# Performance work log

Measured on AMD Instinct MI355X. Metric: run time of the kernel, lower is better.

The kernel has to match this reference:

```python
import jax, jax.numpy as jnp
import numpy as np

NB_CLASSES = 10
EPS = 1e-8  # torch cosine_similarity eps


def gcn_conv(x, W, b, src, dst, n):
    h = x @ W
    deg = jax.ops.segment_sum(jnp.ones_like(src, dtype=h.dtype), dst, num_segments=n) + 1.0
    dinv = deg ** -0.5
    coef = (dinv[src] * dinv[dst])[:, None]
    agg = jax.ops.segment_sum(h[src] * coef, dst, num_segments=n)
    return agg + h * (1.0 / deg)[:, None] + b


def condition_net(e, w_in, b_in, w_hid, b_hid, w_out, b_out):
    # ConditionNet with num_layers=2: input_fc -> elu -> hidden_fc[0] -> elu -> output_fc
    h = jax.nn.elu(e @ w_in + b_in)
    h = jax.nn.elu(h @ w_hid + b_hid)
    return h @ w_out + b_out


def setup_inputs() -> dict:
    key = jax.random.key(0)
    N, E, D, H, T, M = 20000, 320000, 256, 256, 3, 2048
    ks = jax.random.split(key, 24)
    s = 1.0 / np.sqrt(D)
    inp = {
        "x": jax.random.normal(ks[0], (N, D), dtype=jnp.float32),
        "src": jax.random.randint(ks[1], (E,), 0, N, dtype=jnp.int32),
        "dst": jax.random.randint(ks[2], (E,), 0, N, dtype=jnp.int32),
        "idx": jax.random.randint(ks[3], (M,), 0, N, dtype=jnp.int32),
        "labels": jax.random.randint(ks[4], (M,), 0, NB_CLASSES, dtype=jnp.int32),
        "train": 1,
        # 3 GCNConv layers (all D->D, residual structure forces equal widths)
        "gcn_W1": jax.random.normal(ks[5], (D, D), dtype=jnp.float32) * s,
        "gcn_b1": jnp.zeros((D,), dtype=jnp.float32),
        "gcn_W2": jax.random.normal(ks[6], (D, D), dtype=jnp.float32) * s,
        "gcn_b2": jnp.zeros((D,), dtype=jnp.float32),
        "gcn_W3": jax.random.normal(ks[7], (D, D), dtype=jnp.float32) * s,
        "gcn_b3": jnp.zeros((D,), dtype=jnp.float32),
        # T=3 ConditionNets, params stacked on leading axis
        "cn_w_in": jax.random.normal(ks[8], (T, D, H), dtype=jnp.float32) * s,
        "cn_b_in": jnp.zeros((T, H), dtype=jnp.float32),
        "cn_w_hid": jax.random.normal(ks[9], (T, H, H), dtype=jnp.float32) * s,
        "cn_b_hid": jnp.zeros((T, H), dtype=jnp.float32),
        "cn_w_out": jax.random.normal(ks[10], (T, H, D), dtype=jnp.float32) * s,
        "cn_b_out": jnp.zeros((T, D), dtype=jnp.float32),
        # Embed_prompt
        "p_list": jax.random.normal(ks[11], (5, D), dtype=jnp.float32) * s,
        "a_W": jax.random.normal(ks[12], (D, 5), dtype=jnp.float32) * s,
        "a_b": jnp.zeros((5,), dtype=jnp.float32),
        # gcn_weight2 (trainable); weight1 and weight3 are frozen zeros, closed over
        "gcn_weight2": jnp.float32(1.0),
    }
    return inp


def reference(x, src, dst, idx, labels, train,
              gcn_W1, gcn_b1, gcn_W2, gcn_b2, gcn_W3, gcn_b3,
              cn_w_in, cn_b_in, cn_w_hid, cn_b_hid, cn_w_out, cn_b_out,
              p_list, a_W, a_b, gcn_weight2):
    n = x.shape[0]
    origin_x = x
    w1 = jnp.float32(0.0)  # gcn_weight1 (frozen)
    w3 = jnp.float32(0.0)  # gcn_weight3 (frozen)
    T = cn_w_in.shape[0]
    for t in range(T):  # think layers (small static count)
        e1 = gcn_conv(x, gcn_W1, gcn_b1, src, dst, n)
        e2 = gcn_conv(e1, gcn_W2, gcn_b2, src, dst, n) + e1
        e3 = gcn_conv(e2, gcn_W3, gcn_b3, src, dst, n) + e2
        embed = w1 * e1 + gcn_weight2 * e2 + w3 * e3
        prompt = condition_net(embed, cn_w_in[t], cn_b_in[t], cn_w_hid[t], cn_b_hid[t],
                               cn_w_out[t], cn_b_out[t])
        x = prompt * origin_x
    # full gcn(x, edge_index): 3 convs with ELU activation (standard GCN forward)
    h = jax.nn.elu(gcn_conv(x, gcn_W1, gcn_b1, src, dst, n))
    h = jax.nn.elu(gcn_conv(h, gcn_W2, gcn_b2, src, dst, n))
    h = jax.nn.elu(gcn_conv(h, gcn_W3, gcn_b3, src, dst, n))
    # Embed_prompt: attention over 5 learned prompt vectors
    weight = jax.nn.softmax(h @ a_W + a_b, axis=1)  # [N, 5]
    embed = h + weight @ p_list
    rawret = embed[idx]  # [M, D]
    # train==1: class prototypes via scatter-mean over labels
    sums = jax.ops.segment_sum(rawret, labels, num_segments=NB_CLASSES)
    counts = jax.ops.segment_sum(jnp.ones_like(labels, dtype=rawret.dtype), labels,
                                 num_segments=NB_CLASSES)
    ave = sums / jnp.maximum(counts, 1.0)[:, None]  # [C, D]
    # fused cosine similarity: normalize both, one matmul (replaces M*C scalar loop)
    rn = rawret / jnp.maximum(jnp.linalg.norm(rawret, axis=1, keepdims=True), EPS)
    an = ave / jnp.maximum(jnp.linalg.norm(ave, axis=1, keepdims=True), EPS)
    ret = jax.nn.softmax(rn @ an.T, axis=1)  # [M, C]
    return ret
```

## Files before the change

### kernel.cpp

```cpp
#include <hip/hip_runtime.h>
#include <hip/hip_bf16.h>
#include <math.h>

#define NN 20000
#define DD 256
#define EE 320000
#define MM 2048
#define CC 10
#define TT 3

typedef __attribute__((ext_vector_type(8))) short s8v;
typedef __attribute__((ext_vector_type(4))) float f4v;

__device__ unsigned short g_xb[NN * DD];
__device__ unsigned short g_xo[NN * DD];
__device__ unsigned short g_hb[NN * DD];
__device__ unsigned short g_e1b[NN * DD];
__device__ unsigned short g_e2b[NN * DD];
__device__ int   g_cnt[NN];
__device__ int   g_cursor[NN];
__device__ int   g_rowstart[NN + 1];
__device__ float g_dinv[NN];
__device__ float g_invdeg[NN];
__device__ int   g_part[128];
__device__ int2  g_edge[EE];
__device__ float g_sums[CC * DD];
__device__ float g_cntf[CC];
__device__ float g_an[CC * DD];
__device__ unsigned short g_wT1[12 * DD * DD];
__device__ unsigned short g_wT2[12 * DD * DD];

__device__ __forceinline__ float wave_sum(float v) {
#pragma unroll
  for (int off = 32; off > 0; off >>= 1) v += __shfl_xor(v, off);
  return v;
}

__device__ __forceinline__ float eluf(float x) {
  return x > 0.f ? x : expm1f(x);
}

__device__ __forceinline__ float bf2f(unsigned short u) {
  union { unsigned int i; float f; } c;
  c.i = (unsigned int)u << 16;
  return c.f;
}

__device__ __forceinline__ float2 bfpair(unsigned int d) {
  union { unsigned int i; float f; } a, b;
  a.i = d << 16;
  b.i = d & 0xffff0000u;
  return make_float2(a.f, b.f);
}

__device__ __forceinline__ unsigned int packbf(float x, float y) {
  union { __hip_bfloat162 v; unsigned int u; } c;
  c.v = __float22bfloat162_rn(make_float2(x, y));
  return c.u;
}

__device__ __forceinline__ void gl_lds16(const unsigned short* g, unsigned short* l) {
  __builtin_amdgcn_global_load_lds(
      (const __attribute__((address_space(1))) unsigned int*)g,
      (__attribute__((address_space(3))) unsigned int*)l, 16, 0, 0);
}

__global__ void zero_pre() {
  int i = blockIdx.x * blockDim.x + threadIdx.x;
  if (i < NN) { g_cnt[i] = 0; g_cursor[i] = 0; }
  if (i < CC * DD) g_sums[i] = 0.f;
  if (i < CC) g_cntf[i] = 0.f;
}

__global__ void hist_k(const int* __restrict__ dst) {
  int e = blockIdx.x * blockDim.x + threadIdx.x;
  if (e < EE) atomicAdd(&g_cnt[dst[e]], 1);
}

__global__ __launch_bounds__(256) void scanA_k() {
  __shared__ int s[256];
  int t = threadIdx.x;
  int i = blockIdx.x * 256 + t;
  int v = (i < NN) ? g_cnt[i] : 0;
  s[t] = v;
  __syncthreads();
#pragma unroll
  for (int off = 128; off > 0; off >>= 1) {
    if (t < off) s[t] += s[t + off];
    __syncthreads();
  }
  if (t == 0) g_part[blockIdx.x] = s[0];
}

__global__ __launch_bounds__(128) void scanB_k() {
  __shared__ int s[128];
  int t = threadIdx.x;
  int p = (t < 79) ? g_part[t] : 0;
  s[t] = p;
  __syncthreads();
#pragma unroll
  for (int off = 1; off < 128; off <<= 1) {
    int v = (t >= off) ? s[t - off] : 0;
    __syncthreads();
    s[t] += v;
    __syncthreads();
  }
  g_part[t] = s[t] - p;
  if (t == 0) g_rowstart[NN] = EE;
}

__global__ __launch_bounds__(256) void scanC_k() {
  __shared__ int s[256];
  int t = threadIdx.x;
  int i = blockIdx.x * 256 + t;
  int v = (i < NN) ? g_cnt[i] : 0;
  s[t] = v;
  __syncthreads();
#pragma unroll
  for (int off = 1; off < 256; off <<= 1) {
    int x = (t >= off) ? s[t - off] : 0;
    __syncthreads();
    s[t] += x;
    __syncthreads();
  }
  if (i < NN) {
    g_rowstart[i] = g_part[blockIdx.x] + s[t] - v;
    float dg = (float)(v + 1);
    g_invdeg[i] = 1.0f / dg;
    g_dinv[i] = 1.0f / sqrtf(dg);
  }
}

__global__ void fill_k(const int* __restrict__ src, const int* __restrict__ dst) {
  int e = blockIdx.x * blockDim.x + threadIdx.x;
  if (e < EE) {
    int d = dst[e];
    int p = atomicAdd(&g_cursor[d], 1);
    int j = g_rowstart[d] + p;
    int si = src[e];
    float coef = g_dinv[si] * g_dinv[d];
    g_edge[j] = make_int2(si * 512, __float_as_int(coef));
  }
}

__global__ __launch_bounds__(256) void cvt_k(const float* __restrict__ x,
                                             unsigned short* __restrict__ xb) {
  int i = blockIdx.x * blockDim.x + threadIdx.x;
  const float4* x4 = (const float4*)x;
  float4 a = x4[i * 2], b = x4[i * 2 + 1];
  uint4 o;
  o.x = packbf(a.x, a.y);
  o.y = packbf(a.z, a.w);
  o.z = packbf(b.x, b.y);
  o.w = packbf(b.z, b.w);
  ((uint4*)xb)[i] = o;
}

struct WPtrs { const float* p[12]; };

__global__ __launch_bounds__(256) void wprep_k(WPtrs wp) {
  __shared__ float t[64][65];
  int widx = blockIdx.z;
  int kt0 = blockIdx.x * 64, nt0 = blockIdx.y * 64;
  const float* W = wp.p[widx];
  int tid = threadIdx.x;
  int ln = tid & 63, lk = tid >> 6;
  for (int kk = lk; kk < 64; kk += 4)
    t[kk][ln] = W[(size_t)(kt0 + kk) * DD + nt0 + ln];
  __syncthreads();
  for (int nn = lk; nn < 64; nn += 4) {
    float v = t[ln][nn];
    __hip_bfloat16 hb = __float2bfloat16(v);
    float hf = __bfloat162float(hb);
    __hip_bfloat16 lb = __float2bfloat16(v - hf);
    union { __hip_bfloat16 b; unsigned short s; } ch, cl;
    ch.b = hb; cl.b = lb;
    size_t o = (size_t)widx * DD * DD + (size_t)(nt0 + nn) * DD + kt0 + ln;
    g_wT1[o] = ch.s;
    g_wT2[o] = cl.s;
  }
}

union GemmSM {
  unsigned short st[2 * 2048 * 8];
  float ct[128][68];
};

template <int EPI>
__global__ __launch_bounds__(256) void gemm_k(const unsigned short* __restrict__ A,
                                              const unsigned short* __restrict__ B1,
                                              const unsigned short* __restrict__ B2,
                                              unsigned short* __restrict__ C,
                                              const float* __restrict__ bias,
                                              const float* __restrict__ alphap,
                                              const unsigned short* __restrict__ mul) {
  __shared__ GemmSM sm;
  int b = blockIdx.x;
  int xcd = b & 7, off = b >> 3;
  int logical = (xcd < 4) ? xcd * 79 + off : 316 + (xcd - 4) * 78 + off;
  int mblk = logical >> 2, nblk = logical & 3;
  int row0 = mblk * 128, col0 = nblk * 64;

  int tid = threadIdx.x;
  int wv = tid >> 6, lane = tid & 63;
  int wm = wv >> 1, wn = wv & 1;
  int lr = lane & 15, lk = lane >> 4;

  f4v acc[4][2];
#pragma unroll
  for (int i = 0; i < 4; ++i)
#pragma unroll
    for (int j = 0; j < 2; ++j) acc[i][j] = (f4v){0.f, 0.f, 0.f, 0.f};

  auto stage = [&](int buf, int kt) {
    unsigned short* base = sm.st + buf * 16384;
#pragma unroll
    for (int i = 0; i < 8; ++i) {
      int cb = (wv * 8 + i) * 64;
      int c = cb + lane;
      unsigned short* ldst = base + (size_t)cb * 8;
      if (cb < 1024) {
        int row = c >> 3, kc = c & 7;
        int gr = row0 + row;
        gr = gr < NN ? gr : NN - 1;
        gl_lds16(A + (size_t)gr * DD + kt + ((kc ^ (row & 7)) << 3), ldst);
      } else if (cb < 1536) {
        int c2 = c - 1024;
        int col = c2 >> 3, kc = c2 & 7;
        gl_lds16(B1 + (size_t)(col0 + col) * DD + kt + ((kc ^ (col & 7)) << 3), ldst);
      } else {
        int c2 = c - 1536;
        int col = c2 >> 3, kc = c2 & 7;
        gl_lds16(B2 + (size_t)(col0 + col) * DD + kt + ((kc ^ (col & 7)) << 3), ldst);
      }
    }
  };

  stage(0, 0);
  __syncthreads();

  int buf = 0;
#pragma unroll
  for (int t = 0; t < 4; ++t) {
    if (t < 3) stage(buf ^ 1, (t + 1) * 64);
    const unsigned short* base = sm.st + buf * 16384;
#pragma unroll
    for (int ksub = 0; ksub < 2; ++ksub) {
      int kc = ksub * 4 + lk;
      s8v a[4], b1v[2], b2v[2];
#pragma unroll
      for (int mi = 0; mi < 4; ++mi) {
        int row = wm * 64 + mi * 16 + lr;
        a[mi] = *(const s8v*)(base + (row * 8 + (kc ^ (row & 7))) * 8);
      }
#pragma unroll
      for (int nj = 0; nj < 2; ++nj) {
        int col = wn * 32 + nj * 16 + lr;
        int ch = col * 8 + (kc ^ (col & 7));
        b1v[nj] = *(const s8v*)(base + 8192 + ch * 8);
        b2v[nj] = *(const s8v*)(base + 12288 + ch * 8);
      }
#pragma unroll
      for (int mi = 0; mi < 4; ++mi)
#pragma unroll
        for (int nj = 0; nj < 2; ++nj) {
          acc[mi][nj] = __builtin_amdgcn_mfma_f32_16x16x32_bf16(a[mi], b1v[nj], acc[mi][nj], 0, 0, 0);
          acc[mi][nj] = __builtin_amdgcn_mfma_f32_16x16x32_bf16(a[mi], b2v[nj], acc[mi][nj], 0, 0, 0);
        }
    }
    __syncthreads();
    buf ^= 1;
  }

#pragma unroll
  for (int mi = 0; mi < 4; ++mi)
#pragma unroll
    for (int nj = 0; nj < 2; ++nj)
#pragma unroll
      for (int r = 0; r < 4; ++r)
        sm.ct[wm * 64 + mi * 16 + lk * 4 + r][wn * 32 + nj * 16 + lr] = acc[mi][nj][r];
  __syncthreads();

  float alpha = 1.f;
  if (EPI == 1) alpha = alphap ? *alphap : 1.f;
#pragma unroll
  for (int p = 0; p < 4; ++p) {
    int row = p * 32 + (tid >> 3);
    int c0 = (tid & 7) * 8;
    int gr = row0 + row;
    int gc = col0 + c0;
    if (gr < NN) {
      float v[8];
      float4 va = *(float4*)&sm.ct[row][c0];
      float4 vb = *(float4*)&sm.ct[row][c0 + 4];
      v[0] = va.x; v[1] = va.y; v[2] = va.z; v[3] = va.w;
      v[4] = vb.x; v[5] = vb.y; v[6] = vb.z; v[7] = vb.w;
      if (EPI == 1) {
        float4 bv0 = *(const float4*)(bias + gc);
        float4 bv1 = *(const float4*)(bias + gc + 4);
        float bb[8] = {bv0.x, bv0.y, bv0.z, bv0.w, bv1.x, bv1.y, bv1.z, bv1.w};
#pragma unroll
        for (int i = 0; i < 8; ++i) v[i] = eluf(fmaf(alpha, v[i], bb[i]));
      } else if (EPI == 2) {
        float4 bv0 = *(const float4*)(bias + gc);
        float4 bv1 = *(const float4*)(bias + gc + 4);
        float bb[8] = {bv0.x, bv0.y, bv0.z, bv0.w, bv1.x, bv1.y, bv1.z, bv1.w};
        uint4 mu = *(const uint4*)(mul + (size_t)gr * DD + gc);
        float2 m0 = bfpair(mu.x), m1 = bfpair(mu.y), m2 = bfpair(mu.z), m3 = bfpair(mu.w);
        float mm[8] = {m0.x, m0.y, m1.x, m1.y, m2.x, m2.y, m3.x, m3.y};
#pragma unroll
        for (int i = 0; i < 8; ++i) v[i] = (v[i] + bb[i]) * mm[i];
      }
      uint4 o;
      o.x = packbf(v[0], v[1]);
      o.y = packbf(v[2], v[3]);
      o.z = packbf(v[4], v[5]);
      o.w = packbf(v[6], v[7]);
      *(uint4*)(C + (size_t)gr * DD + gc) = o;
    }
  }
}

template <int RES>
__device__ __forceinline__ float4 agg_row_b(int row, int lane,
                                            const unsigned short* __restrict__ h,
                                            const float* __restrict__ bias,
                                            const unsigned short* __restrict__ res) {
  const char* hb = (const char*)h;
  int lo = lane * 8;
  float4 a = make_float4(0.f, 0.f, 0.f, 0.f);
  int s = g_rowstart[row], e = g_rowstart[row + 1];
  int j = s;
  for (; j + 16 <= e; j += 16) {
    int2 E[16];
    uint2 v[16];
#pragma unroll
    for (int u = 0; u < 16; ++u) E[u] = g_edge[j + u];
#pragma unroll
    for (int u = 0; u < 16; ++u) v[u] = *(const uint2*)(hb + E[u].x + lo);
#pragma unroll
    for (int u = 0; u < 16; ++u) {
      float c = __int_as_float(E[u].y);
      float2 p0 = bfpair(v[u].x), p1 = bfpair(v[u].y);
      a.x = fmaf(c, p0.x, a.x); a.y = fmaf(c, p0.y, a.y);
      a.z = fmaf(c, p1.x, a.z); a.w = fmaf(c, p1.y, a.w);
    }
  }
  for (; j + 4 <= e; j += 4) {
    int2 E[4];
    uint2 v[4];
#pragma unroll
    for (int u = 0; u < 4; ++u) E[u] = g_edge[j + u];
#pragma unroll
    for (int u = 0; u < 4; ++u) v[u] = *(const uint2*)(hb + E[u].x + lo);
#pragma unroll
    for (int u = 0; u < 4; ++u) {
      float c = __int_as_float(E[u].y);
      float2 p0 = bfpair(v[u].x), p1 = bfpair(v[u].y);
      a.x = fmaf(c, p0.x, a.x); a.y = fmaf(c, p0.y, a.y);
      a.z = fmaf(c, p1.x, a.z); a.w = fmaf(c, p1.y, a.w);
    }
  }
  for (; j < e; ++j) {
    int2 E0 = g_edge[j];
    uint2 v0 = *(const uint2*)(hb + E0.x + lo);
    float c = __int_as_float(E0.y);
    float2 p0 = bfpair(v0.x), p1 = bfpair(v0.y);
    a.x = fmaf(c, p0.x, a.x); a.y = fmaf(c, p0.y, a.y);
    a.z = fmaf(c, p1.x, a.z); a.w = fmaf(c, p1.y, a.w);
  }
  float idg = g_invdeg[row];
  uint2 hv = *(const uint2*)(hb + row * 512 + lo);
  float2 h0 = bfpair(hv.x), h1 = bfpair(hv.y);
  float4 bv = ((const float4*)bias)[lane];
  float4 o;
  o.x = a.x + h0.x * idg + bv.x;
  o.y = a.y + h0.y * idg + bv.y;
  o.z = a.z + h1.x * idg + bv.z;
  o.w = a.w + h1.y * idg + bv.w;
  if (RES) {
    uint2 rv = *(const uint2*)((const char*)res + row * 512 + lo);
    float2 r0 = bfpair(rv.x), r1 = bfpair(rv.y);
    o.x += r0.x; o.y += r0.y; o.z += r1.x; o.w += r1.y;
  }
  return o;
}

template <int ELU, int RES>
__global__ __launch_bounds__(256) void agg_k(const unsigned short* __restrict__ h,
                                             const float* __restrict__ bias,
                                             const unsigned short* __restrict__ res,
                                             unsigned short* __restrict__ out) {
  int row = (blockIdx.x * 256 + threadIdx.x) >> 6;
  int lane = threadIdx.x & 63;
  float4 o = agg_row_b<RES>(row, lane, h, bias, res);
  if (ELU) {
    o.x = eluf(o.x); o.y = eluf(o.y); o.z = eluf(o.z); o.w = eluf(o.w);
  }
  ((uint2*)out)[(size_t)row * 64 + lane] = make_uint2(packbf(o.x, o.y), packbf(o.z, o.w));
}

__global__ __launch_bounds__(256) void aggattn_k(const unsigned short* __restrict__ h,
                                                 const float* __restrict__ bias,
                                                 const float* __restrict__ aW,
                                                 const float* __restrict__ ab,
                                                 const float* __restrict__ plist,
                                                 unsigned short* __restrict__ out) {
  int row = (blockIdx.x * 256 + threadIdx.x) >> 6;
  int lane = threadIdx.x & 63;
  float4 o = agg_row_b<0>(row, lane, h, bias, nullptr);
  o.x = eluf(o.x); o.y = eluf(o.y); o.z = eluf(o.z); o.w = eluf(o.w);
  int d = lane * 4;
  float lg[5];
#pragma unroll
  for (int k = 0; k < 5; ++k) {
    float p = o.x * aW[(d + 0) * 5 + k] + o.y * aW[(d + 1) * 5 + k] +
              o.z * aW[(d + 2) * 5 + k] + o.w * aW[(d + 3) * 5 + k];
    lg[k] = wave_sum(p) + ab[k];
  }
  float mx = lg[0];
#pragma unroll
  for (int k = 1; k < 5; ++k) mx = fmaxf(mx, lg[k]);
  float w[5], sum = 0.f;
#pragma unroll
  for (int k = 0; k < 5; ++k) { w[k] = expf(lg[k] - mx); sum += w[k]; }
  float inv = 1.f / sum;
#pragma unroll
  for (int k = 0; k < 5; ++k) {
    float wk = w[k] * inv;
    float4 pv = ((const float4*)plist)[k * 64 + lane];
    o.x = fmaf(wk, pv.x, o.x);
    o.y = fmaf(wk, pv.y, o.y);
    o.z = fmaf(wk, pv.z, o.z);
    o.w = fmaf(wk, pv.w, o.w);
  }
  ((uint2*)out)[(size_t)row * 64 + lane] = make_uint2(packbf(o.x, o.y), packbf(o.z, o.w));
}

__global__ __launch_bounds__(256) void proto_k(const unsigned short* __restrict__ embed,
                                               const int* __restrict__ idxp,
                                               const int* __restrict__ labels) {
  __shared__ float sums[CC][DD];
  __shared__ float cnts[CC];
  int t = threadIdx.x;
#pragma unroll
  for (int c = 0; c < CC; ++c) sums[c][t] = 0.f;
  if (t < CC) cnts[t] = 0.f;
  __syncthreads();
  int m0 = blockIdx.x * 32;
  for (int r0 = 0; r0 < 32; r0 += 4) {
    int i4[4], l4[4];
    float v[4];
#pragma unroll
    for (int u = 0; u < 4; ++u) {
      int m = m0 + r0 + u;
      i4[u] = idxp[m];
      l4[u] = labels[m];
    }
#pragma unroll
    for (int u = 0; u < 4; ++u) v[u] = bf2f(embed[(size_t)i4[u] * DD + t]);
#pragma unroll
    for (int u = 0; u < 4; ++u) sums[l4[u]][t] += v[u];
    if (t == 0) {
#pragma unroll
      for (int u = 0; u < 4; ++u) cnts[l4[u]] += 1.f;
    }
  }
  __syncthreads();
#pragma unroll
  for (int c = 0; c < CC; ++c) atomicAdd(&g_sums[c * DD + t], sums[c][t]);
  if (t < CC) atomicAdd(&g_cntf[t], cnts[t]);
}

__global__ void protonorm_k() {
  __shared__ float red[4];
  int t = threadIdx.x;
  int lane = t & 63, w = t >> 6;
  for (int c = 0; c < CC; ++c) {
    float v = g_sums[c * DD + t] / fmaxf(g_cntf[c], 1.0f);
    float sq = wave_sum(v * v);
    if (lane == 0) red[w] = sq;
    __syncthreads();
    float tot = red[0] + red[1] + red[2] + red[3];
    float nrm = fmaxf(sqrtf(tot), 1e-8f);
    g_an[c * DD + t] = v / nrm;
    __syncthreads();
  }
}

__global__ __launch_bounds__(256) void cos_k(const unsigned short* __restrict__ embed,
                                             const int* __restrict__ idxp,
                                             float* __restrict__ out) {
  int wid = (blockIdx.x * 256 + threadIdx.x) >> 6;
  int lane = threadIdx.x & 63;
  if (wid >= MM) return;
  int row = idxp[wid];
  uint2 rv = ((const uint2*)embed)[(size_t)row * 64 + lane];
  float2 r0 = bfpair(rv.x), r1 = bfpair(rv.y);
  float4 r = make_float4(r0.x, r0.y, r1.x, r1.y);
  float n = wave_sum(r.x * r.x + r.y * r.y + r.z * r.z + r.w * r.w);
  float rnf = 1.0f / fmaxf(sqrtf(n), 1e-8f);
  float lg[CC];
#pragma unroll
  for (int c = 0; c < CC; ++c) {
    float4 a = ((const float4*)g_an)[c * 64 + lane];
    float p = r.x * a.x + r.y * a.y + r.z * a.z + r.w * a.w;
    lg[c] = wave_sum(p) * rnf;
  }
  float mx = lg[0];
#pragma unroll
  for (int c = 1; c < CC; ++c) mx = fmaxf(mx, lg[c]);
  float s = 0.f, w[CC];
#pragma unroll
  for (int c = 0; c < CC; ++c) { w[c] = expf(lg[c] - mx); s += w[c]; }
  float inv = 1.f / s;
#pragma unroll
  for (int c = 0; c < CC; ++c)
    if (lane == c) out[(size_t)wid * CC + c] = w[c] * inv;
}

extern "C" void kernel_launch(void* const* d_in, const int* in_sizes, int n_in,
                              void* d_out, int out_size, void* d_ws, size_t ws_size,
                              hipStream_t stream) {
  (void)in_sizes; (void)n_in; (void)d_ws; (void)ws_size; (void)out_size;
  const float* x      = (const float*)d_in[0];
  const int*   src    = (const int*)d_in[1];
  const int*   dst    = (const int*)d_in[2];
  const int*   idx    = (const int*)d_in[3];
  const int*   labels = (const int*)d_in[4];
  const float* W1 = (const float*)d_in[6];
  const float* b1 = (const float*)d_in[7];
  const float* W2 = (const float*)d_in[8];
  const float* b2 = (const float*)d_in[9];
  const float* W3 = (const float*)d_in[10];
  const float* b3 = (const float*)d_in[11];
  const float* cw_in  = (const float*)d_in[12];
  const float* cb_in  = (const float*)d_in[13];
  const float* cw_hid = (const float*)d_in[14];
  const float* cb_hid = (const float*)d_in[15];
  const float* cw_out = (const float*)d_in[16];
  const float* cb_out = (const float*)d_in[17];
  const float* plist  = (const float*)d_in[18];
  const float* aW     = (const float*)d_in[19];
  const float* ab     = (const float*)d_in[20];
  const float* w2s    = (const float*)d_in[21];
  float* out = (float*)d_out;

  unsigned short *xb, *xo, *hb, *e1b, *e2b, *wt1, *wt2;
  hipGetSymbolAddress((void**)&xb,  HIP_SYMBOL(g_xb));
  hipGetSymbolAddress((void**)&xo,  HIP_SYMBOL(g_xo));
  hipGetSymbolAddress((void**)&hb,  HIP_SYMBOL(g_hb));
  hipGetSymbolAddress((void**)&e1b, HIP_SYMBOL(g_e1b));
  hipGetSymbolAddress((void**)&e2b, HIP_SYMBOL(g_e2b));
  hipGetSymbolAddress((void**)&wt1, HIP_SYMBOL(g_wT1));
  hipGetSymbolAddress((void**)&wt2, HIP_SYMBOL(g_wT2));

  auto WT1 = [&](int w) { return (const unsigned short*)(wt1 + (size_t)w * DD * DD); };
  auto WT2 = [&](int w) { return (const unsigned short*)(wt2 + (size_t)w * DD * DD); };

  zero_pre<<<79, 256, 0, stream>>>();
  hist_k<<<1250, 256, 0, stream>>>(dst);
  scanA_k<<<79, 256, 0, stream>>>();
  scanB_k<<<1, 128, 0, stream>>>();
  scanC_k<<<79, 256, 0, stream>>>();
  fill_k<<<1250, 256, 0, stream>>>(src, dst);
  cvt_k<<<2500, 256, 0, stream>>>(x, xb);

  WPtrs wp;
  wp.p[0] = W1; wp.p[1] = W2; wp.p[2] = W3;
  for (int t = 0; t < 3; ++t) {
    wp.p[3 + t] = cw_in  + (size_t)t * DD * DD;
    wp.p[6 + t] = cw_hid + (size_t)t * DD * DD;
    wp.p[9 + t] = cw_out + (size_t)t * DD * DD;
  }
  wprep_k<<<dim3(4, 4, 12), 256, 0, stream>>>(wp);

  const int GG = 628;
  const unsigned short* xin = xb;
  for (int t = 0; t < TT; ++t) {
    gemm_k<0><<<GG, 256, 0, stream>>>(xin, WT1(0), WT2(0), hb, nullptr, nullptr, nullptr);
    agg_k<0, 0><<<5000, 256, 0, stream>>>(hb, b1, nullptr, e1b);
    gemm_k<0><<<GG, 256, 0, stream>>>(e1b, WT1(1), WT2(1), hb, nullptr, nullptr, nullptr);
    agg_k<0, 1><<<5000, 256, 0, stream>>>(hb, b2, e1b, e2b);
    gemm_k<1><<<GG, 256, 0, stream>>>(e2b, WT1(3 + t), WT2(3 + t), e1b,
                                      cb_in + (size_t)t * DD, w2s, nullptr);
    gemm_k<1><<<GG, 256, 0, stream>>>(e1b, WT1(6 + t), WT2(6 + t), hb,
                                      cb_hid + (size_t)t * DD, nullptr, nullptr);
    gemm_k<2><<<GG, 256, 0, stream>>>(hb, WT1(9 + t), WT2(9 + t), xo,
                                      cb_out + (size_t)t * DD, nullptr, xb);
    xin = xo;
  }

  gemm_k<0><<<GG, 256, 0, stream>>>(xin, WT1(0), WT2(0), hb, nullptr, nullptr, nullptr);
  agg_k<1, 0><<<5000, 256, 0, stream>>>(hb, b1, nullptr, e1b);
  gemm_k<0><<<GG, 256, 0, stream>>>(e1b, WT1(1), WT2(1), hb, nullptr, nullptr, nullptr);
  agg_k<1, 0><<<5000, 256, 0, stream>>>(hb, b2, nullptr, e2b);
  gemm_k<0><<<GG, 256, 0, stream>>>(e2b, WT1(2), WT2(2), hb, nullptr, nullptr, nullptr);
  aggattn_k<<<5000, 256, 0, stream>>>(hb, b3, aW, ab, plist, e2b);

  proto_k<<<64, 256, 0, stream>>>(e2b, idx, labels);
  protonorm_k<<<1, 256, 0, stream>>>();
  cos_k<<<512, 256, 0, stream>>>(e2b, idx, out);
}
```

Before: 631.6 us.

## Halve GEMM M-tile and drop low-bf16 weight split for ConditionNet GEMMs

The GEMM block tile shrinks from 128 to 64 rows, doubling the grid to 1252 blocks and cutting per-block LDS use, which should help occupancy and load balance. A new SPLIT template parameter lets the ConditionNet GEMMs skip the second low-order bf16 weight pass, halving their MFMA work and B-tile staging. The risk is lower precision in the ConditionNet path, since weights are now bf16-rounded only, and more total A re-reads from the smaller tile.

```diff
diff --git a/kernel.cpp b/kernel.cpp
--- a/kernel.cpp
+++ b/kernel.cpp
@@ -181,12 +181,13 @@
   }
 }
 
+template <int SPLIT>
 union GemmSM {
-  unsigned short st[2 * 2048 * 8];
-  float ct[128][68];
+  unsigned short st[2][(1024 + 512 * SPLIT) * 8];
+  float ct[64][68];
 };
 
-template <int EPI>
+template <int EPI, int SPLIT>
 __global__ __launch_bounds__(256) void gemm_k(const unsigned short* __restrict__ A,
                                               const unsigned short* __restrict__ B1,
                                               const unsigned short* __restrict__ B2,
@@ -194,44 +195,48 @@
                                               const float* __restrict__ bias,
                                               const float* __restrict__ alphap,
                                               const unsigned short* __restrict__ mul) {
-  __shared__ GemmSM sm;
+  __shared__ GemmSM<SPLIT> sm;
+  constexpr int CB = 1024 + 512 * SPLIT;
   int b = blockIdx.x;
   int xcd = b & 7, off = b >> 3;
-  int logical = (xcd < 4) ? xcd * 79 + off : 316 + (xcd - 4) * 78 + off;
+  int logical = (xcd < 4) ? xcd * 157 + off : 628 + (xcd - 4) * 156 + off;
   int mblk = logical >> 2, nblk = logical & 3;
-  int row0 = mblk * 128, col0 = nblk * 64;
+  int row0 = mblk * 64, col0 = nblk * 64;
 
   int tid = threadIdx.x;
   int wv = tid >> 6, lane = tid & 63;
   int wm = wv >> 1, wn = wv & 1;
   int lr = lane & 15, lk = lane >> 4;
 
-  f4v acc[4][2];
-#pragma unroll
-  for (int i = 0; i < 4; ++i)
+  f4v acc[2][2];
+#pragma unroll
+  for (int i = 0; i < 2; ++i)
 #pragma unroll
     for (int j = 0; j < 2; ++j) acc[i][j] = (f4v){0.f, 0.f, 0.f, 0.f};
 
   auto stage = [&](int buf, int kt) {
-    unsigned short* base = sm.st + buf * 16384;
-#pragma unroll
-    for (int i = 0; i < 8; ++i) {
-      int cb = (wv * 8 + i) * 64;
+    unsigned short* base = sm.st[buf];
+#pragma unroll
+    for (int i = 0; i < CB / 256; ++i) {
+      int cb = (wv * (CB / 256) + i) * 64;
       int c = cb + lane;
       unsigned short* ldst = base + (size_t)cb * 8;
-      if (cb < 1024) {
-        int row = c >> 3, kc = c & 7;
+      if (c < 512) {
+        int row = c >> 3, pos = c & 7;
+        int kc = pos ^ (row & 7);
         int gr = row0 + row;
         gr = gr < NN ? gr : NN - 1;
-        gl_lds16(A + (size_t)gr * DD + kt + ((kc ^ (row & 7)) << 3), ldst);
-      } else if (cb < 1536) {
+        gl_lds16(A + (size_t)gr * DD + kt + kc * 8, ldst);
+      } else if (c < 1024) {
+        int c2 = c - 512;
+        int col = c2 >> 3, pos = c2 & 7;
+        int kc = pos ^ (col & 7);
+        gl_lds16(B1 + (size_t)(col0 + col) * DD + kt + kc * 8, ldst);
+      } else {
         int c2 = c - 1024;
-        int col = c2 >> 3, kc = c2 & 7;
-        gl_lds16(B1 + (size_t)(col0 + col) * DD + kt + ((kc ^ (col & 7)) << 3), ldst);
-      } else {
-        int c2 = c - 1536;
-        int col = c2 >> 3, kc = c2 & 7;
-        gl_lds16(B2 + (size_t)(col0 + col) * DD + kt + ((kc ^ (col & 7)) << 3), ldst);
+        int col = c2 >> 3, pos = c2 & 7;
+        int kc = pos ^ (col & 7);
+        gl_lds16(B2 + (size_t)(col0 + col) * DD + kt + kc * 8, ldst);
       }
     }
   };
@@ -243,29 +248,30 @@
 #pragma unroll
   for (int t = 0; t < 4; ++t) {
     if (t < 3) stage(buf ^ 1, (t + 1) * 64);
-    const unsigned short* base = sm.st + buf * 16384;
+    const unsigned short* base = sm.st[buf];
 #pragma unroll
     for (int ksub = 0; ksub < 2; ++ksub) {
       int kc = ksub * 4 + lk;
-      s8v a[4], b1v[2], b2v[2];
-#pragma unroll
-      for (int mi = 0; mi < 4; ++mi) {
-        int row = wm * 64 + mi * 16 + lr;
+      s8v a[2], b1v[2], b2v[2];
+#pragma unroll
+      for (int mi = 0; mi < 2; ++mi) {
+        int row = wm * 32 + mi * 16 + lr;
         a[mi] = *(const s8v*)(base + (row * 8 + (kc ^ (row & 7))) * 8);
       }
 #pragma unroll
       for (int nj = 0; nj < 2; ++nj) {
         int col = wn * 32 + nj * 16 + lr;
         int ch = col * 8 + (kc ^ (col & 7));
-        b1v[nj] = *(const s8v*)(base + 8192 + ch * 8);
-        b2v[nj] = *(const s8v*)(base + 12288 + ch * 8);
+        b1v[nj] = *(const s8v*)(base + (512 + ch) * 8);
+        if (SPLIT) b2v[nj] = *(const s8v*)(base + (1024 + ch) * 8);
       }
 #pragma unroll
-      for (int mi = 0; mi < 4; ++mi)
+      for (int mi = 0; mi < 2; ++mi)
 #pragma unroll
         for (int nj = 0; nj < 2; ++nj) {
           acc[mi][nj] = __builtin_amdgcn_mfma_f32_16x16x32_bf16(a[mi], b1v[nj], acc[mi][nj], 0, 0, 0);
-          acc[mi][nj] = __builtin_amdgcn_mfma_f32_16x16x32_bf16(a[mi], b2v[nj], acc[mi][nj], 0, 0, 0);
+          if (SPLIT)
+            acc[mi][nj] = __builtin_amdgcn_mfma_f32_16x16x32_bf16(a[mi], b2v[nj], acc[mi][nj], 0, 0, 0);
         }
     }
     __syncthreads();
@@ -273,18 +279,18 @@
   }
 
 #pragma unroll
-  for (int mi = 0; mi < 4; ++mi)
+  for (int mi = 0; mi < 2; ++mi)
 #pragma unroll
     for (int nj = 0; nj < 2; ++nj)
 #pragma unroll
       for (int r = 0; r < 4; ++r)
-        sm.ct[wm * 64 + mi * 16 + lk * 4 + r][wn * 32 + nj * 16 + lr] = acc[mi][nj][r];
+        sm.ct[wm * 32 + mi * 16 + lk * 4 + r][wn * 32 + nj * 16 + lr] = acc[mi][nj][r];
   __syncthreads();
 
   float alpha = 1.f;
   if (EPI == 1) alpha = alphap ? *alphap : 1.f;
 #pragma unroll
-  for (int p = 0; p < 4; ++p) {
+  for (int p = 0; p < 2; ++p) {
     int row = p * 32 + (tid >> 3);
     int c0 = (tid & 7) * 8;
     int gr = row0 + row;
@@ -575,27 +581,27 @@
   }
   wprep_k<<<dim3(4, 4, 12), 256, 0, stream>>>(wp);
 
-  const int GG = 628;
+  const int GG = 1252;
   const unsigned short* xin = xb;
   for (int t = 0; t < TT; ++t) {
-    gemm_k<0><<<GG, 256, 0, stream>>>(xin, WT1(0), WT2(0), hb, nullptr, nullptr, nullptr);
+    gemm_k<0, 1><<<GG, 256, 0, stream>>>(xin, WT1(0), WT2(0), hb, nullptr, nullptr, nullptr);
     agg_k<0, 0><<<5000, 256, 0, stream>>>(hb, b1, nullptr, e1b);
-    gemm_k<0><<<GG, 256, 0, stream>>>(e1b, WT1(1), WT2(1), hb, nullptr, nullptr, nullptr);
+    gemm_k<0, 1><<<GG, 256, 0, stream>>>(e1b, WT1(1), WT2(1), hb, nullptr, nullptr, nullptr);
     agg_k<0, 1><<<5000, 256, 0, stream>>>(hb, b2, e1b, e2b);
-    gemm_k<1><<<GG, 256, 0, stream>>>(e2b, WT1(3 + t), WT2(3 + t), e1b,
-                                      cb_in + (size_t)t * DD, w2s, nullptr);
-    gemm_k<1><<<GG, 256, 0, stream>>>(e1b, WT1(6 + t), WT2(6 + t), hb,
-                                      cb_hid + (size_t)t * DD, nullptr, nullptr);
-    gemm_k<2><<<GG, 256, 0, stream>>>(hb, WT1(9 + t), WT2(9 + t), xo,
-                                      cb_out + (size_t)t * DD, nullptr, xb);
+    gemm_k<1, 0><<<GG, 256, 0, stream>>>(e2b, WT1(3 + t), WT1(3 + t), e1b,
+                                         cb_in + (size_t)t * DD, w2s, nullptr);
+    gemm_k<1, 0><<<GG, 256, 0, stream>>>(e1b, WT1(6 + t), WT1(6 + t), hb,
+                                         cb_hid + (size_t)t * DD, nullptr, nullptr);
+    gemm_k<2, 0><<<GG, 256, 0, stream>>>(hb, WT1(9 + t), WT1(9 + t), xo,
+                                         cb_out + (size_t)t * DD, nullptr, xb);
     xin = xo;
   }
 
-  gemm_k<0><<<GG, 256, 0, stream>>>(xin, WT1(0), WT2(0), hb, nullptr, nullptr, nullptr);
+  gemm_k<0, 1><<<GG, 256, 0, stream>>>(xin, WT1(0), WT2(0), hb, nullptr, nullptr, nullptr);
   agg_k<1, 0><<<5000, 256, 0, stream>>>(hb, b1, nullptr, e1b);
-  gemm_k<0><<<GG, 256, 0, stream>>>(e1b, WT1(1), WT2(1), hb, nullptr, nullptr, nullptr);
+  gemm_k<0, 1><<<GG, 256, 0, stream>>>(e1b, WT1(1), WT2(1), hb, nullptr, nullptr, nullptr);
   agg_k<1, 0><<<5000, 256, 0, stream>>>(hb, b2, nullptr, e2b);
-  gemm_k<0><<<GG, 256, 0, stream>>>(e2b, WT1(2), WT2(2), hb, nullptr, nullptr, nullptr);
+  gemm_k<0, 1><<<GG, 256, 0, stream>>>(e2b, WT1(2), WT2(2), hb, nullptr, nullptr, nullptr);
   aggattn_k<<<5000, 256, 0, stream>>>(hb, b3, aW, ab, plist, e2b);
 
   proto_k<<<64, 256, 0, stream>>>(e2b, idx, labels);
```

Measured after the change: 579.8 us. 1.09x faster.
